# Performance work log

Measured on AMD Instinct MI355X. Metric: run time of the kernel, lower is better.

Reference implementation:

```python
import jax, jax.numpy as jnp
import numpy as np

B, S, HID = 2, 1024, 4096
H, KV, D = 32, 8, 128
EPS = 1e-6
ROPE_THETA = 1000000.0


def _make_freqs_cis(seq_len, head_dim, theta):
    inv_freq = 1.0 / (theta ** (jnp.arange(0, head_dim, 2, dtype=jnp.float32) / head_dim))
    ang = jnp.arange(seq_len, dtype=jnp.float32)[:, None] * inv_freq[None, :]  # [S, D/2]
    emb = jnp.concatenate([ang, ang], axis=-1)                                 # [S, D]
    cos, sin = jnp.cos(emb), jnp.sin(emb)
    return jnp.stack([cos, sin, -sin], axis=0)                                 # [3, S, D]


def setup_inputs() -> dict:
    key = jax.random.key(0)
    ks = jax.random.split(key, 8)
    scale = 0.02
    return {
        "hidden_states": jax.random.normal(ks[0], (B, S, HID), dtype=jnp.float32),
        "freqs_cis": _make_freqs_cis(S, D, ROPE_THETA),
        "Wq": jax.random.normal(ks[1], (H * D, HID), dtype=jnp.float32) * scale,
        "Wk": jax.random.normal(ks[2], (KV * D, HID), dtype=jnp.float32) * scale,
        "Wv": jax.random.normal(ks[3], (KV * D, HID), dtype=jnp.float32) * scale,
        "Wo": jax.random.normal(ks[4], (HID, H * D), dtype=jnp.float32) * scale,
        "q_norm_w": jnp.ones((D,), jnp.float32) + jax.random.normal(ks[5], (D,), jnp.float32) * scale,
        "k_norm_w": jnp.ones((D,), jnp.float32) + jax.random.normal(ks[6], (D,), jnp.float32) * scale,
    }


def _rmsnorm(x, w):
    # per-head RMSNorm over last dim (rms_norm_add=False -> plain weight multiply)
    return x * jax.lax.rsqrt(jnp.mean(x * x, axis=-1, keepdims=True) + EPS) * w


def _rope(x, cos, sin, nsin):
    # matches apply_rope: e = x*cos; e[:half] += x[half:]*nsin; e[half:] += x[:half]*sin
    half = x.shape[-1] // 2
    e = x * cos
    lo = e[..., :half] + x[..., half:] * nsin[..., :half]
    hi = e[..., half:] + x[..., :half] * sin[..., half:]
    return jnp.concatenate([lo, hi], axis=-1)


def reference(hidden_states, freqs_cis, Wq, Wk, Wv, Wo, q_norm_w, k_norm_w):
    b, s, _ = hidden_states.shape
    # QKV projections (no bias)
    q = jnp.einsum("bsh,oh->bso", hidden_states, Wq).reshape(b, s, H, D).transpose(0, 2, 1, 3)
    k = jnp.einsum("bsh,oh->bso", hidden_states, Wk).reshape(b, s, KV, D).transpose(0, 2, 1, 3)
    v = jnp.einsum("bsh,oh->bso", hidden_states, Wv).reshape(b, s, KV, D).transpose(0, 2, 1, 3)
    # per-head RMSNorm (Qwen3 'gemma3' q/k norms)
    q = _rmsnorm(q, q_norm_w)
    k = _rmsnorm(k, k_norm_w)
    # RoPE
    cos, sin, nsin = freqs_cis[0], freqs_cis[1], freqs_cis[2]  # [S, D] each, broadcast over (b, heads)
    q = _rope(q, cos, sin, nsin)
    k = _rope(k, cos, sin, nsin)
    # GQA: repeat kv heads to match query heads (repeat_interleave dim=1)
    rep = H // KV
    k = jnp.repeat(k, rep, axis=1)
    v = jnp.repeat(v, rep, axis=1)
    # SDPA (no mask, past_key_value=None path)
    scale = D ** -0.5
    attn = jax.nn.softmax(jnp.einsum("bhqd,bhkd->bhqk", q, k) * scale, axis=-1)
    out = jnp.einsum("bhqk,bhkd->bhqd", attn, v)
    out = out.transpose(0, 2, 1, 3).reshape(b, s, H * D)
    return jnp.einsum("bsi,hi->bsh", out, Wo)
```

## Files before the change

kernel.cpp:

```cpp
#include <hip/hip_runtime.h>


typedef __attribute__((ext_vector_type(8))) short s8v;
typedef __attribute__((ext_vector_type(4))) float f4v;
typedef __attribute__((ext_vector_type(8))) unsigned short u8v;
typedef __attribute__((ext_vector_type(4))) float float4v;
typedef __attribute__((ext_vector_type(2))) float float2v;
typedef unsigned short us;

#define SB() __builtin_amdgcn_sched_barrier(0)

__device__ __forceinline__ void BARRIER() {
  asm volatile("" ::: "memory");
  __builtin_amdgcn_s_barrier();
  asm volatile("" ::: "memory");
}

__device__ __forceinline__ us f2b(float f) {
  unsigned u = __builtin_bit_cast(unsigned, f);
  u += 0x7fffu + ((u >> 16) & 1u);
  return (us)(u >> 16);
}
__device__ __forceinline__ float b2f(us h) {
  return __builtin_bit_cast(float, (unsigned)h << 16);
}

__device__ __forceinline__ void gload16(const void* g, void* l) {
  __builtin_amdgcn_global_load_lds(
      (const __attribute__((address_space(1))) unsigned int*)g,
      (__attribute__((address_space(3))) unsigned int*)l, 16, 0, 0);
}

__global__ __launch_bounds__(256) void cvt_all_k(const float* __restrict__ h,
                                                 const float* __restrict__ wq,
                                                 const float* __restrict__ wk,
                                                 const float* __restrict__ wv,
                                                 us* __restrict__ dst) {
  long blk = blockIdx.x;
  const float* src;
  long off;
  if (blk < 4096)        { src = h;  off = 0; }
  else if (blk < 12288)  { src = wq; off = 4096; }
  else if (blk < 14336)  { src = wk; off = 12288; }
  else                   { src = wv; off = 14336; }
  long i = (blk - off) * 2048 + (long)threadIdx.x * 8;
  long o = blk * 2048 + (long)threadIdx.x * 8;
  float4v a = *(const float4v*)(src + i);
  float4v b = *(const float4v*)(src + i + 4);
  u8v v;
  v[0] = f2b(a[0]); v[1] = f2b(a[1]); v[2] = f2b(a[2]); v[3] = f2b(a[3]);
  v[4] = f2b(b[0]); v[5] = f2b(b[1]); v[6] = f2b(b[2]); v[7] = f2b(b[3]);
  *(u8v*)(dst + o) = v;
}

template <int AH, bool F32OUT, bool CVTTAIL>
__global__ __launch_bounds__(512, 2) void gemm8p(const us* __restrict__ A,
                                                 const us* __restrict__ W,
                                                 void* __restrict__ Cv,
                                                 int K, int nkt, int ldc,
                                                 int cm, int cn, int ncn,
                                                 int nGemm,
                                                 const float* __restrict__ csrc,
                                                 us* __restrict__ cdst) {
  if constexpr (CVTTAIL) {
    if ((int)blockIdx.x >= nGemm) {
      long c = (long)((int)blockIdx.x - nGemm) * 512 + threadIdx.x;
      for (; c < 2097152; c += 64 * 512) {
        long i = c * 8;
        float4v x = *(const float4v*)(csrc + i);
        float4v y = *(const float4v*)(csrc + i + 4);
        u8v v;
        v[0] = f2b(x[0]); v[1] = f2b(x[1]); v[2] = f2b(x[2]); v[3] = f2b(x[3]);
        v[4] = f2b(y[0]); v[5] = f2b(y[1]); v[6] = f2b(y[2]); v[7] = f2b(y[3]);
        *(u8v*)(cdst + i) = v;
      }
      return;
    }
  }

  constexpr int FR = AH / 32;
  constexpr int LA = AH / 64;
  constexpr int VM = 2 * LA + 2;

  __shared__ __align__(16) us Ah[2][2][AH * 64];
  __shared__ __align__(16) us Bh[2][2][128 * 64];
  const int tid = threadIdx.x, lane = tid & 63, w = tid >> 6;
  const int wr = w >> 2, wc = w & 3;
  const int lr = lane & 15, lg = lane >> 4;

  const int xcd = (int)blockIdx.x & 7;
  const int i2 = (int)blockIdx.x >> 3;
  const int im = i2 % cm, itn = i2 / cm;
  const long m0 = (long)((xcd / ncn) * cm + im) * (2 * AH);
  const long n0 = (long)((xcd % ncn) * cn + itn) * 256;

  const int rA0 = tid >> 3;
  const int sc0 = ((tid & 7) ^ (rA0 & 7)) << 3;

#define STGH(dst, src, LOADS)                                           \
  do {                                                                  \
    const us* _s = (src);                                               \
    us* _d = (dst);                                                     \
    _Pragma("unroll") for (int l = 0; l < (LOADS); ++l)                 \
      gload16(_s + (long)(rA0 + l * 64) * K + sc0, _d + (l * 512 + tid) * 8); \
  } while (0)

  const us* Asrc = A + m0 * K;
  const us* Bsrc = W + n0 * K;
  const long hKA = (long)AH * K;
  const long hKB = (long)128 * K;

  const int ra = wr * (AH / 2) + lr, rb = wc * 32 + lr;
  const int offA0 = ra * 64 + ((lg ^ (ra & 7)) << 3);
  const int offA1 = ra * 64 + (((4 + lg) ^ (ra & 7)) << 3);
  const int offB0 = rb * 64 + ((lg ^ (rb & 7)) << 3);
  const int offB1 = rb * 64 + (((4 + lg) ^ (rb & 7)) << 3);

  f4v acc[2 * FR][4];
#pragma unroll
  for (int i = 0; i < 2 * FR; ++i)
#pragma unroll
    for (int j = 0; j < 4; ++j) acc[i][j] = (f4v){0.f, 0.f, 0.f, 0.f};

  const int nk = nkt;

  STGH(Ah[0][0], Asrc, LA);
  STGH(Bh[0][0], Bsrc, 2);
  STGH(Bh[0][1], Bsrc + hKB, 2);
  STGH(Ah[0][1], Asrc + hKA, LA);
  STGH(Ah[1][0], Asrc + 64, LA);
  STGH(Bh[1][1], Bsrc + hKB + 64, 2);
  STGH(Ah[1][1], Asrc + hKA + 64, LA);
  asm volatile("s_waitcnt vmcnt(%0)" :: "i"(VM) : "memory");
  BARRIER();

  s8v a[FR][2], b0[2][2], b1[2][2];

#define RD_A(H)                                                         \
  _Pragma("unroll") for (int f = 0; f < FR; ++f) {                      \
    a[f][0] = *(const s8v*)(&Ah[d][H][offA0 + f * 1024]);               \
    a[f][1] = *(const s8v*)(&Ah[d][H][offA1 + f * 1024]);               \
  }
#define RD_B(BB, H)                                                     \
  _Pragma("unroll") for (int g = 0; g < 2; ++g) {                       \
    BB[g][0] = *(const s8v*)(&Bh[d][H][offB0 + g * 1024]);              \
    BB[g][1] = *(const s8v*)(&Bh[d][H][offB1 + g * 1024]);              \
  }
#define QUAD(QM, QN, BB)                                                \
  __builtin_amdgcn_s_setprio(1);                                        \
  _Pragma("unroll") for (int f = 0; f < FR; ++f)                        \
  _Pragma("unroll") for (int g = 0; g < 2; ++g) {                       \
    f4v t = acc[QM * FR + f][QN * 2 + g];                               \
    t = __builtin_amdgcn_mfma_f32_16x16x32_bf16(a[f][0], BB[g][0], t, 0, 0, 0); \
    t = __builtin_amdgcn_mfma_f32_16x16x32_bf16(a[f][1], BB[g][1], t, 0, 0, 0); \
    acc[QM * FR + f][QN * 2 + g] = t;                                   \
  }                                                                     \
  __builtin_amdgcn_s_setprio(0);
#define PREMFMA()                                                       \
  BARRIER();                                                            \
  asm volatile("s_waitcnt lgkmcnt(0)" ::: "memory");                    \
  SB();

  for (int kt = 0; kt < nk; ++kt) {
    const int d = kt & 1;
    const long kb2 = (long)(kt + 2) * 64;
    const bool p1 = (kt + 1 < nk), p2 = (kt + 2 < nk);

    RD_A(0)
    RD_B(b0, 0)
    if (p1) STGH(Bh[d ^ 1][0], Bsrc + (long)(kt + 1) * 64, 2);
    PREMFMA()
    QUAD(0, 0, b0)
    SB(); BARRIER();

    RD_B(b1, 1)
    if (p2) STGH(Ah[d][0], Asrc + kb2, LA);
    PREMFMA()
    QUAD(0, 1, b1)
    SB(); BARRIER();

    RD_A(1)
    if (p2) STGH(Bh[d][1], Bsrc + hKB + kb2, 2);
    PREMFMA()
    QUAD(1, 1, b1)
    SB(); BARRIER();

    if (p2) STGH(Ah[d][1], Asrc + hKA + kb2, LA);
    PREMFMA()
    QUAD(1, 0, b0)
    SB();
    if (p2) asm volatile("s_waitcnt vmcnt(%0)" :: "i"(VM) : "memory");
    else    asm volatile("s_waitcnt vmcnt(0)" ::: "memory");
    BARRIER();
  }

#pragma unroll
  for (int qm = 0; qm < 2; ++qm)
#pragma unroll
    for (int f = 0; f < FR; ++f) {
      long row = m0 + qm * AH + wr * (AH / 2) + f * 16 + lg * 4;
#pragma unroll
      for (int qn = 0; qn < 2; ++qn)
#pragma unroll
        for (int g = 0; g < 2; ++g) {
          long col = n0 + qn * 128 + wc * 32 + g * 16 + lr;
          f4v v = acc[qm * FR + f][qn * 2 + g];
          if constexpr (F32OUT) {
            float* C = (float*)Cv;
#pragma unroll
            for (int r = 0; r < 4; ++r) C[(row + r) * ldc + col] = v[r];
          } else {
            us* C = (us*)Cv;
#pragma unroll
            for (int r = 0; r < 4; ++r) C[(row + r) * ldc + col] = f2b(v[r]);
          }
        }
    }
#undef STGH
#undef RD_A
#undef RD_B
#undef QUAD
#undef PREMFMA
}

__global__ __launch_bounds__(256) void rms_rope_k(us* __restrict__ qkv,
                                                  const float* __restrict__ fc,
                                                  const float* __restrict__ qw,
                                                  const float* __restrict__ kw) {
  int idx = blockIdx.x * 4 + (threadIdx.x >> 6);
  int lane = threadIdx.x & 63;
  int head = idx % 40;
  int row = idx / 40;
  int s = row & 1023;
  us* p;
  const float* w;
  if (head < 32) { p = qkv + (long)row * 6144 + head * 128; w = qw; }
  else           { p = qkv + (long)row * 6144 + 4096 + (head - 32) * 128; w = kw; }

  unsigned v = ((const unsigned*)p)[lane];
  float x0 = b2f((us)(v & 0xffff)), x1 = b2f((us)(v >> 16));
  float ss = x0 * x0 + x1 * x1;
#pragma unroll
  for (int off = 32; off; off >>= 1) ss += __shfl_xor(ss, off);
  float r = rsqrtf(ss * (1.0f / 128.0f) + 1e-6f);
  float2v wv = ((const float2v*)w)[lane];
  float y0 = x0 * r * wv[0], y1 = x1 * r * wv[1];
  float py0 = __shfl(y0, lane ^ 32);
  float py1 = __shfl(y1, lane ^ 32);
  float2v cv = ((const float2v*)(fc + (long)s * 128))[lane];
  const float* sbase = (lane < 32) ? (fc + 2 * 1024 * 128) : (fc + 1024 * 128);
  float2v sv = ((const float2v*)(sbase + (long)s * 128))[lane];
  float e0 = y0 * cv[0] + py0 * sv[0];
  float e1 = y1 * cv[1] + py1 * sv[1];
  ((unsigned*)p)[lane] = (unsigned)f2b(e0) | ((unsigned)f2b(e1) << 16);
}

__global__ __launch_bounds__(256) void attn_k(const us* __restrict__ qkv,
                                              us* __restrict__ ao) {
  __shared__ us Kt[64 * 128];
  __shared__ us Vt[128 * 72];
  __shared__ us Pl[4 * 1024];

  const int bid = blockIdx.x;
  const int qt = bid & 15;
  const int h = (bid >> 4) & 31;
  const int b = bid >> 9;
  const int kvh = h >> 2;
  const int tid = threadIdx.x, lane = tid & 63, w = tid >> 6;
  const int lr = lane & 15, lg = lane >> 4;

  const us* Qb =
      qkv + (long)(b * 1024 + qt * 64 + w * 16 + lr) * 6144 + h * 128;
  s8v qf[4];
#pragma unroll
  for (int ks = 0; ks < 4; ++ks) qf[ks] = *(const s8v*)(Qb + ks * 32 + lg * 8);

  f4v o[8];
#pragma unroll
  for (int n = 0; n < 8; ++n) o[n] = (f4v){0.f, 0.f, 0.f, 0.f};
  float m[4], l[4];
#pragma unroll
  for (int r = 0; r < 4; ++r) { m[r] = -1e30f; l[r] = 0.f; }

  const float SL = 0.08838834764831845f * 1.4426950408889634f;
  const long krow = (long)b * 1024 * 6144 + 4096 + kvh * 128;
  const long vrow = (long)b * 1024 * 6144 + 5120 + kvh * 128;

  for (int kt = 0; kt < 16; ++kt) {
    __syncthreads();
#pragma unroll
    for (int t = 0; t < 4; ++t) {
      int c = t * 256 + tid;
      int row = c >> 4;
      int sc = (c & 15) ^ (row & 7);
      gload16(qkv + krow + (long)(kt * 64 + row) * 6144 + sc * 8, &Kt[c * 8]);
    }
#pragma unroll
    for (int t = 0; t < 4; ++t) {
      int c = t * 256 + tid;
      int key = c & 63;
      int d0 = (c >> 6) * 8;
      s8v v = *(const s8v*)(qkv + vrow + (long)(kt * 64 + key) * 6144 + d0);
#pragma unroll
      for (int i = 0; i < 8; ++i) Vt[(d0 + i) * 72 + key] = (us)v[i];
    }
    __syncthreads();

    f4v sacc[4];
#pragma unroll
    for (int j = 0; j < 4; ++j) sacc[j] = (f4v){0.f, 0.f, 0.f, 0.f};
    __builtin_amdgcn_s_setprio(1);
#pragma unroll
    for (int ks = 0; ks < 4; ++ks) {
#pragma unroll
      for (int j = 0; j < 4; ++j) {
        int key = j * 16 + lr;
        s8v kf = *(const s8v*)&Kt[key * 128 + (((ks * 64 + lg * 16) ^ ((key & 7) << 4)) >> 1)];
        sacc[j] = __builtin_amdgcn_mfma_f32_16x16x32_bf16(qf[ks], kf, sacc[j], 0, 0, 0);
      }
    }
    __builtin_amdgcn_s_setprio(0);

    float sm[4];
#pragma unroll
    for (int r = 0; r < 4; ++r)
      sm[r] = fmaxf(fmaxf(sacc[0][r], sacc[1][r]), fmaxf(sacc[2][r], sacc[3][r]));
#pragma unroll
    for (int off = 1; off < 16; off <<= 1)
#pragma unroll
      for (int r = 0; r < 4; ++r) sm[r] = fmaxf(sm[r], __shfl_xor(sm[r], off));
    float alpha[4];
#pragma unroll
    for (int r = 0; r < 4; ++r) {
      float nm = fmaxf(m[r], sm[r] * SL);
      alpha[r] = exp2f(m[r] - nm);
      m[r] = nm;
      l[r] *= alpha[r];
    }
#pragma unroll
    for (int n = 0; n < 8; ++n)
#pragma unroll
      for (int r = 0; r < 4; ++r) o[n][r] *= alpha[r];

    us* pw = Pl + w * 1024;
#pragma unroll
    for (int j = 0; j < 4; ++j)
#pragma unroll
      for (int r = 0; r < 4; ++r) {
        float p = exp2f(sacc[j][r] * SL - m[r]);
        l[r] += p;
        int prow = lg * 4 + r, pcol = j * 16 + lr;
        pw[(prow * 128 + ((pcol * 2) ^ ((prow & 7) << 4))) >> 1] = f2b(p);
      }

    __builtin_amdgcn_s_setprio(1);
#pragma unroll
    for (int ks = 0; ks < 2; ++ks) {
      int bo = ks * 64 + lg * 16;
      s8v pf = *(const s8v*)&Pl[w * 1024 + ((lr * 128 + (bo ^ ((lr & 7) << 4))) >> 1)];
#pragma unroll
      for (int n = 0; n < 8; ++n) {
        s8v vf = *(const s8v*)&Vt[(n * 16 + lr) * 72 + ks * 32 + lg * 8];
        o[n] = __builtin_amdgcn_mfma_f32_16x16x32_bf16(pf, vf, o[n], 0, 0, 0);
      }
    }
    __builtin_amdgcn_s_setprio(0);
  }

#pragma unroll
  for (int off = 1; off < 16; off <<= 1)
#pragma unroll
    for (int r = 0; r < 4; ++r) l[r] += __shfl_xor(l[r], off);
  float inv[4];
#pragma unroll
  for (int r = 0; r < 4; ++r) inv[r] = 1.f / l[r];
  const long ob = (long)(b * 1024 + qt * 64 + w * 16) * 4096 + h * 128;
#pragma unroll
  for (int n = 0; n < 8; ++n)
#pragma unroll
    for (int r = 0; r < 4; ++r)
      ao[ob + (long)(lg * 4 + r) * 4096 + n * 16 + lr] = f2b(o[n][r] * inv[r]);
}

extern "C" void kernel_launch(void* const* d_in, const int* in_sizes, int n_in,
                              void* d_out, int out_size, void* d_ws, size_t ws_size,
                              hipStream_t stream) {
  const float* hidden = (const float*)d_in[0];
  const float* fc     = (const float*)d_in[1];
  const float* Wq     = (const float*)d_in[2];
  const float* Wk     = (const float*)d_in[3];
  const float* Wv     = (const float*)d_in[4];
  const float* Wo     = (const float*)d_in[5];
  const float* qw     = (const float*)d_in[6];
  const float* kw     = (const float*)d_in[7];

  us* hb  = (us*)d_ws;
  us* wb  = hb + (long)2048 * 4096;
  us* wbo = wb + (long)6144 * 4096;
  us* qkv = wbo + (long)4096 * 4096;
  us* ao  = qkv + (long)2048 * 6144;

  cvt_all_k<<<16384, 256, 0, stream>>>(hidden, Wq, Wk, Wv, hb);

  gemm8p<128, false, true><<<256, 512, 0, stream>>>(
      hb, wb, qkv, 4096, 64, 6144, 4, 6, 4, 192, Wo, wbo);

  rms_rope_k<<<20480, 256, 0, stream>>>(qkv, fc, qw, kw);

  attn_k<<<1024, 256, 0, stream>>>(qkv, ao);

  gemm8p<64, true, false><<<256, 512, 0, stream>>>(
      ao, wbo, d_out, 4096, 64, 4096, 8, 4, 4, 256, nullptr, nullptr);
}
```

Baseline: 345.2 us.

## Software-pipeline LDS fragment reads across GEMM k-tiles with partial lgkmcnt waits

After: 581.8 us. +68.5%, slower.

```diff
diff --git a/kernel.cpp b/kernel.cpp
--- a/kernel.cpp
+++ b/kernel.cpp
@@ -80,7 +80,6 @@
 
   constexpr int FR = AH / 32;
   constexpr int LA = AH / 64;
-  constexpr int VM = 2 * LA + 2;
 
   __shared__ __align__(16) us Ah[2][2][AH * 64];
   __shared__ __align__(16) us Bh[2][2][128 * 64];
@@ -124,6 +123,31 @@
 
   const int nk = nkt;
 
+  s8v a0[FR][2], a1[FR][2], b0A[2][2], b0B[2][2], b1[2][2];
+
+#define RD_A(AA, D, H)                                                  \
+  _Pragma("unroll") for (int f = 0; f < FR; ++f) {                      \
+    AA[f][0] = *(const s8v*)(&Ah[D][H][offA0 + f * 1024]);              \
+    AA[f][1] = *(const s8v*)(&Ah[D][H][offA1 + f * 1024]);              \
+  }
+#define RD_B(BB, D, H)                                                  \
+  _Pragma("unroll") for (int g = 0; g < 2; ++g) {                       \
+    BB[g][0] = *(const s8v*)(&Bh[D][H][offB0 + g * 1024]);              \
+    BB[g][1] = *(const s8v*)(&Bh[D][H][offB1 + g * 1024]);              \
+  }
+#define QUAD(AA, BB, QM, QN)                                            \
+  __builtin_amdgcn_s_setprio(1);                                        \
+  _Pragma("unroll") for (int f = 0; f < FR; ++f)                        \
+  _Pragma("unroll") for (int g = 0; g < 2; ++g) {                       \
+    f4v t = acc[QM * FR + f][QN * 2 + g];                               \
+    t = __builtin_amdgcn_mfma_f32_16x16x32_bf16(AA[f][0], BB[g][0], t, 0, 0, 0); \
+    t = __builtin_amdgcn_mfma_f32_16x16x32_bf16(AA[f][1], BB[g][1], t, 0, 0, 0); \
+    acc[QM * FR + f][QN * 2 + g] = t;                                   \
+  }                                                                     \
+  __builtin_amdgcn_s_setprio(0);
+#define LGKMW(N) asm volatile("s_waitcnt lgkmcnt(%0)" :: "i"(N) : "memory")
+#define VMCNTW(N) asm volatile("s_waitcnt vmcnt(%0)" :: "i"(N) : "memory")
+
   STGH(Ah[0][0], Asrc, LA);
   STGH(Bh[0][0], Bsrc, 2);
   STGH(Bh[0][1], Bsrc + hKB, 2);
@@ -131,67 +155,56 @@
   STGH(Ah[1][0], Asrc + 64, LA);
   STGH(Bh[1][1], Bsrc + hKB + 64, 2);
   STGH(Ah[1][1], Asrc + hKA + 64, LA);
-  asm volatile("s_waitcnt vmcnt(%0)" :: "i"(VM) : "memory");
+  VMCNTW(2 * LA + 2);
   BARRIER();
-
-  s8v a[FR][2], b0[2][2], b1[2][2];
-
-#define RD_A(H)                                                         \
-  _Pragma("unroll") for (int f = 0; f < FR; ++f) {                      \
-    a[f][0] = *(const s8v*)(&Ah[d][H][offA0 + f * 1024]);               \
-    a[f][1] = *(const s8v*)(&Ah[d][H][offA1 + f * 1024]);               \
-  }
-#define RD_B(BB, H)                                                     \
-  _Pragma("unroll") for (int g = 0; g < 2; ++g) {                       \
-    BB[g][0] = *(const s8v*)(&Bh[d][H][offB0 + g * 1024]);              \
-    BB[g][1] = *(const s8v*)(&Bh[d][H][offB1 + g * 1024]);              \
-  }
-#define QUAD(QM, QN, BB)                                                \
-  __builtin_amdgcn_s_setprio(1);                                        \
-  _Pragma("unroll") for (int f = 0; f < FR; ++f)                        \
-  _Pragma("unroll") for (int g = 0; g < 2; ++g) {                       \
-    f4v t = acc[QM * FR + f][QN * 2 + g];                               \
-    t = __builtin_amdgcn_mfma_f32_16x16x32_bf16(a[f][0], BB[g][0], t, 0, 0, 0); \
-    t = __builtin_amdgcn_mfma_f32_16x16x32_bf16(a[f][1], BB[g][1], t, 0, 0, 0); \
-    acc[QM * FR + f][QN * 2 + g] = t;                                   \
-  }                                                                     \
-  __builtin_amdgcn_s_setprio(0);
-#define PREMFMA()                                                       \
-  BARRIER();                                                            \
-  asm volatile("s_waitcnt lgkmcnt(0)" ::: "memory");                    \
-  SB();
-
-  for (int kt = 0; kt < nk; ++kt) {
-    const int d = kt & 1;
-    const long kb2 = (long)(kt + 2) * 64;
-    const bool p1 = (kt + 1 < nk), p2 = (kt + 2 < nk);
-
-    RD_A(0)
-    RD_B(b0, 0)
-    if (p1) STGH(Bh[d ^ 1][0], Bsrc + (long)(kt + 1) * 64, 2);
-    PREMFMA()
-    QUAD(0, 0, b0)
-    SB(); BARRIER();
-
-    RD_B(b1, 1)
-    if (p2) STGH(Ah[d][0], Asrc + kb2, LA);
-    PREMFMA()
-    QUAD(0, 1, b1)
-    SB(); BARRIER();
-
-    RD_A(1)
-    if (p2) STGH(Bh[d][1], Bsrc + hKB + kb2, 2);
-    PREMFMA()
-    QUAD(1, 1, b1)
-    SB(); BARRIER();
-
-    if (p2) STGH(Ah[d][1], Asrc + hKA + kb2, LA);
-    PREMFMA()
-    QUAD(1, 0, b0)
-    SB();
-    if (p2) asm volatile("s_waitcnt vmcnt(%0)" :: "i"(VM) : "memory");
-    else    asm volatile("s_waitcnt vmcnt(0)" ::: "memory");
-    BARRIER();
+  RD_A(a0, 0, 0);
+  RD_B(b0A, 0, 0);
+
+#define TILE(KT, D, B0CUR, B0NXT)                                       \
+  do {                                                                  \
+    const int kt = (KT);                                                \
+    const long kb2 = (long)(kt + 2) * 64;                               \
+    const bool p1 = (kt + 1 < nk), p2 = (kt + 2 < nk);                  \
+                                        \
+    RD_B(b1, D, 1);                                                     \
+    if (p1) STGH(Bh[(D) ^ 1][0], Bsrc + (long)(kt + 1) * 64, 2);        \
+    BARRIER();                                                          \
+    LGKMW(4); SB();                                                     \
+    QUAD(a0, B0CUR, 0, 0)                                               \
+    SB(); BARRIER();                                                    \
+                                        \
+    RD_A(a1, D, 1);                                                     \
+    if (p2) STGH(Ah[D][0], Asrc + kb2, LA);                             \
+    BARRIER();                                                          \
+    LGKMW(2 * FR); SB();                                                \
+    QUAD(a0, b1, 0, 1)                                                  \
+    SB(); BARRIER();                                                    \
+                                        \
+    if (p2) STGH(Bh[D][1], Bsrc + hKB + kb2, 2);                        \
+    BARRIER();                                                          \
+    LGKMW(0); SB();                                                     \
+    QUAD(a1, b1, 1, 1)                                                  \
+    SB(); BARRIER();                                                    \
+               \
+    if (p2)      { VMCNTW(LA + 2); }                                    \
+    else         { VMCNTW(0); }                                         \
+    if (p2) STGH(Ah[D][1], Asrc + hKA + kb2, LA);                       \
+    BARRIER();                                                          \
+    if (p1) {                                                           \
+      RD_A(a0, (D) ^ 1, 0);                                             \
+      RD_B(B0NXT, (D) ^ 1, 0);                                          \
+      LGKMW(2 * FR + 4);                                                \
+    } else {                                                            \
+      LGKMW(0);                                                         \
+    }                                                                   \
+    SB();                                                               \
+    QUAD(a1, B0CUR, 1, 0)                                               \
+    SB(); BARRIER();                                                    \
+  } while (0)
+
+  for (int kt2 = 0; kt2 < nk; kt2 += 2) {
+    TILE(kt2, 0, b0A, b0B);
+    TILE(kt2 + 1, 1, b0B, b0A);
   }
 
 #pragma unroll
@@ -220,7 +233,9 @@
 #undef RD_A
 #undef RD_B
 #undef QUAD
-#undef PREMFMA
+#undef TILE
+#undef LGKMW
+#undef VMCNTW
 }
 
 __global__ __launch_bounds__(256) void rms_rope_k(us* __restrict__ qkv,
```

## Double-buffer GEMM LDS fragment reads to overlap with MFMA quadrants

Applied to the files above, without the earlier changes.

Result: slower. 379.0 us (+9.8%).

```diff
diff --git a/kernel.cpp b/kernel.cpp
--- a/kernel.cpp
+++ b/kernel.cpp
@@ -54,7 +54,7 @@
 }
 
 template <int AH, bool F32OUT, bool CVTTAIL>
-__global__ __launch_bounds__(512, 2) void gemm8p(const us* __restrict__ A,
+__global__ __launch_bounds__(512, 1) void gemm8p(const us* __restrict__ A,
                                                  const us* __restrict__ W,
                                                  void* __restrict__ Cv,
                                                  int K, int nkt, int ldc,
@@ -80,7 +80,6 @@
 
   constexpr int FR = AH / 32;
   constexpr int LA = AH / 64;
-  constexpr int VM = 2 * LA + 2;
 
   __shared__ __align__(16) us Ah[2][2][AH * 64];
   __shared__ __align__(16) us Bh[2][2][128 * 64];
@@ -124,6 +123,31 @@
 
   const int nk = nkt;
 
+  s8v a0[FR][2], a1[FR][2], b0[2][2], b1[2][2];
+
+#define RD_A(AA, D, H)                                                  \
+  _Pragma("unroll") for (int f = 0; f < FR; ++f) {                      \
+    AA[f][0] = *(const s8v*)(&Ah[D][H][offA0 + f * 1024]);              \
+    AA[f][1] = *(const s8v*)(&Ah[D][H][offA1 + f * 1024]);              \
+  }
+#define RD_B(BB, D, H)                                                  \
+  _Pragma("unroll") for (int g = 0; g < 2; ++g) {                       \
+    BB[g][0] = *(const s8v*)(&Bh[D][H][offB0 + g * 1024]);              \
+    BB[g][1] = *(const s8v*)(&Bh[D][H][offB1 + g * 1024]);              \
+  }
+#define QUAD(AA, BB, QM, QN)                                            \
+  __builtin_amdgcn_s_setprio(1);                                        \
+  _Pragma("unroll") for (int f = 0; f < FR; ++f)                        \
+  _Pragma("unroll") for (int g = 0; g < 2; ++g) {                       \
+    f4v t = acc[QM * FR + f][QN * 2 + g];                               \
+    t = __builtin_amdgcn_mfma_f32_16x16x32_bf16(AA[f][0], BB[g][0], t, 0, 0, 0); \
+    t = __builtin_amdgcn_mfma_f32_16x16x32_bf16(AA[f][1], BB[g][1], t, 0, 0, 0); \
+    acc[QM * FR + f][QN * 2 + g] = t;                                   \
+  }                                                                     \
+  __builtin_amdgcn_s_setprio(0);
+#define LGKMW(N) asm volatile("s_waitcnt lgkmcnt(%0)" :: "i"(N) : "memory")
+#define VMCNTW(N) asm volatile("s_waitcnt vmcnt(%0)" :: "i"(N) : "memory")
+
   STGH(Ah[0][0], Asrc, LA);
   STGH(Bh[0][0], Bsrc, 2);
   STGH(Bh[0][1], Bsrc + hKB, 2);
@@ -131,66 +155,50 @@
   STGH(Ah[1][0], Asrc + 64, LA);
   STGH(Bh[1][1], Bsrc + hKB + 64, 2);
   STGH(Ah[1][1], Asrc + hKA + 64, LA);
-  asm volatile("s_waitcnt vmcnt(%0)" :: "i"(VM) : "memory");
+  VMCNTW(2 * LA + 2);
   BARRIER();
-
-  s8v a[FR][2], b0[2][2], b1[2][2];
-
-#define RD_A(H)                                                         \
-  _Pragma("unroll") for (int f = 0; f < FR; ++f) {                      \
-    a[f][0] = *(const s8v*)(&Ah[d][H][offA0 + f * 1024]);               \
-    a[f][1] = *(const s8v*)(&Ah[d][H][offA1 + f * 1024]);               \
-  }
-#define RD_B(BB, H)                                                     \
-  _Pragma("unroll") for (int g = 0; g < 2; ++g) {                       \
-    BB[g][0] = *(const s8v*)(&Bh[d][H][offB0 + g * 1024]);              \
-    BB[g][1] = *(const s8v*)(&Bh[d][H][offB1 + g * 1024]);              \
-  }
-#define QUAD(QM, QN, BB)                                                \
-  __builtin_amdgcn_s_setprio(1);                                        \
-  _Pragma("unroll") for (int f = 0; f < FR; ++f)                        \
-  _Pragma("unroll") for (int g = 0; g < 2; ++g) {                       \
-    f4v t = acc[QM * FR + f][QN * 2 + g];                               \
-    t = __builtin_amdgcn_mfma_f32_16x16x32_bf16(a[f][0], BB[g][0], t, 0, 0, 0); \
-    t = __builtin_amdgcn_mfma_f32_16x16x32_bf16(a[f][1], BB[g][1], t, 0, 0, 0); \
-    acc[QM * FR + f][QN * 2 + g] = t;                                   \
-  }                                                                     \
-  __builtin_amdgcn_s_setprio(0);
-#define PREMFMA()                                                       \
-  BARRIER();                                                            \
-  asm volatile("s_waitcnt lgkmcnt(0)" ::: "memory");                    \
-  SB();
+  RD_A(a0, 0, 0);
+  RD_B(b0, 0, 0);
 
   for (int kt = 0; kt < nk; ++kt) {
     const int d = kt & 1;
     const long kb2 = (long)(kt + 2) * 64;
     const bool p1 = (kt + 1 < nk), p2 = (kt + 2 < nk);
 
-    RD_A(0)
-    RD_B(b0, 0)
+    RD_B(b1, d, 1);
     if (p1) STGH(Bh[d ^ 1][0], Bsrc + (long)(kt + 1) * 64, 2);
-    PREMFMA()
-    QUAD(0, 0, b0)
+    BARRIER();
+    LGKMW(4); SB();
+    QUAD(a0, b0, 0, 0)
     SB(); BARRIER();
 
-    RD_B(b1, 1)
+    RD_A(a1, d, 1);
     if (p2) STGH(Ah[d][0], Asrc + kb2, LA);
-    PREMFMA()
-    QUAD(0, 1, b1)
+    BARRIER();
+    LGKMW(2 * FR); SB();
+    QUAD(a0, b1, 0, 1)
     SB(); BARRIER();
 
-    RD_A(1)
     if (p2) STGH(Bh[d][1], Bsrc + hKB + kb2, 2);
-    PREMFMA()
-    QUAD(1, 1, b1)
+    BARRIER();
+    LGKMW(0); SB();
+    QUAD(a1, b1, 1, 1)
     SB(); BARRIER();
 
+    if (p2)      { VMCNTW(LA + 2); }
+    else         { VMCNTW(0); }
     if (p2) STGH(Ah[d][1], Asrc + hKA + kb2, LA);
-    PREMFMA()
-    QUAD(1, 0, b0)
+    BARRIER();
+    if (p1) {
+      RD_A(a0, d ^ 1, 0);
+      LGKMW(2 * FR);
+    } else {
+      LGKMW(0);
+    }
     SB();
-    if (p2) asm volatile("s_waitcnt vmcnt(%0)" :: "i"(VM) : "memory");
-    else    asm volatile("s_waitcnt vmcnt(0)" ::: "memory");
+    QUAD(a1, b0, 1, 0)
+    SB();
+    if (p1) RD_B(b0, d ^ 1, 0);
     BARRIER();
   }
 
@@ -220,7 +228,8 @@
 #undef RD_A
 #undef RD_B
 #undef QUAD
-#undef PREMFMA
+#undef LGKMW
+#undef VMCNTW
 }
 
 __global__ __launch_bounds__(256) void rms_rope_k(us* __restrict__ qkv,
```

## Fuse Q RMSNorm+RoPE into attention, pack V transpose stores, relax GEMM sched barriers

Applied to the files above, without the earlier changes.

After: 337.5 us. 1.02x faster.

```diff
diff --git a/kernel.cpp b/kernel.cpp
--- a/kernel.cpp
+++ b/kernel.cpp
@@ -171,24 +171,23 @@
     if (p1) STGH(Bh[d ^ 1][0], Bsrc + (long)(kt + 1) * 64, 2);
     PREMFMA()
     QUAD(0, 0, b0)
-    SB(); BARRIER();
+    BARRIER();
 
     RD_B(b1, 1)
     if (p2) STGH(Ah[d][0], Asrc + kb2, LA);
     PREMFMA()
     QUAD(0, 1, b1)
-    SB(); BARRIER();
+    BARRIER();
 
     RD_A(1)
     if (p2) STGH(Bh[d][1], Bsrc + hKB + kb2, 2);
     PREMFMA()
     QUAD(1, 1, b1)
-    SB(); BARRIER();
+    BARRIER();
 
     if (p2) STGH(Ah[d][1], Asrc + hKA + kb2, LA);
     PREMFMA()
     QUAD(1, 0, b0)
-    SB();
     if (p2) asm volatile("s_waitcnt vmcnt(%0)" :: "i"(VM) : "memory");
     else    asm volatile("s_waitcnt vmcnt(0)" ::: "memory");
     BARRIER();
@@ -225,17 +224,14 @@
 
 __global__ __launch_bounds__(256) void rms_rope_k(us* __restrict__ qkv,
                                                   const float* __restrict__ fc,
-                                                  const float* __restrict__ qw,
                                                   const float* __restrict__ kw) {
   int idx = blockIdx.x * 4 + (threadIdx.x >> 6);
   int lane = threadIdx.x & 63;
-  int head = idx % 40;
-  int row = idx / 40;
+  int head = idx & 7;
+  int row = idx >> 3;
   int s = row & 1023;
-  us* p;
-  const float* w;
-  if (head < 32) { p = qkv + (long)row * 6144 + head * 128; w = qw; }
-  else           { p = qkv + (long)row * 6144 + 4096 + (head - 32) * 128; w = kw; }
+  us* p = qkv + (long)row * 6144 + 4096 + head * 128;
+  const float* w = kw;
 
   unsigned v = ((const unsigned*)p)[lane];
   float x0 = b2f((us)(v & 0xffff)), x1 = b2f((us)(v >> 16));
@@ -256,7 +252,9 @@
 }
 
 __global__ __launch_bounds__(256) void attn_k(const us* __restrict__ qkv,
-                                              us* __restrict__ ao) {
+                                              us* __restrict__ ao,
+                                              const float* __restrict__ fc,
+                                              const float* __restrict__ qw) {
   __shared__ us Kt[64 * 128];
   __shared__ us Vt[128 * 72];
   __shared__ us Pl[4 * 1024];
@@ -269,11 +267,40 @@
   const int tid = threadIdx.x, lane = tid & 63, w = tid >> 6;
   const int lr = lane & 15, lg = lane >> 4;
 
-  const us* Qb =
-      qkv + (long)(b * 1024 + qt * 64 + w * 16 + lr) * 6144 + h * 128;
+  const int srow = qt * 64 + w * 16 + lr;
+  const us* Qb = qkv + (long)(b * 1024 + srow) * 6144 + h * 128;
+  s8v qr[4];
+#pragma unroll
+  for (int ks = 0; ks < 4; ++ks) qr[ks] = *(const s8v*)(Qb + ks * 32 + lg * 8);
+
+  float ssq = 0.f;
+#pragma unroll
+  for (int ks = 0; ks < 4; ++ks)
+#pragma unroll
+    for (int j = 0; j < 8; ++j) {
+      float x = b2f((us)qr[ks][j]);
+      ssq += x * x;
+    }
+  ssq += __shfl_xor(ssq, 16);
+  ssq += __shfl_xor(ssq, 32);
+  const float rr = rsqrtf(ssq * (1.0f / 128.0f) + 1e-6f);
+
+  const float* cosp = fc + (long)srow * 128;
+  const float* sinp = fc + 1024 * 128 + (long)srow * 128;
   s8v qf[4];
 #pragma unroll
-  for (int ks = 0; ks < 4; ++ks) qf[ks] = *(const s8v*)(Qb + ks * 32 + lg * 8);
+  for (int ks = 0; ks < 4; ++ks) {
+    const int d0 = ks * 32 + lg * 8;
+    const int dp = d0 ^ 64;
+    const float sgn = (ks < 2) ? -1.f : 1.f;
+#pragma unroll
+    for (int j = 0; j < 8; ++j) {
+      float y  = b2f((us)qr[ks][j])     * rr * qw[d0 + j];
+      float yp = b2f((us)qr[ks ^ 2][j]) * rr * qw[dp + j];
+      float e = y * cosp[d0 + j] + yp * sgn * sinp[d0 + j];
+      qf[ks][j] = (short)f2b(e);
+    }
+  }
 
   f4v o[8];
 #pragma unroll
@@ -296,13 +323,18 @@
       gload16(qkv + krow + (long)(kt * 64 + row) * 6144 + sc * 8, &Kt[c * 8]);
     }
 #pragma unroll
-    for (int t = 0; t < 4; ++t) {
+    for (int t = 0; t < 2; ++t) {
       int c = t * 256 + tid;
-      int key = c & 63;
-      int d0 = (c >> 6) * 8;
-      s8v v = *(const s8v*)(qkv + vrow + (long)(kt * 64 + key) * 6144 + d0);
-#pragma unroll
-      for (int i = 0; i < 8; ++i) Vt[(d0 + i) * 72 + key] = (us)v[i];
+      int kp = c & 31;
+      int d0 = (c >> 5) * 8;
+      const us* vsrc = qkv + vrow + (long)(kt * 64) * 6144 + d0;
+      s8v va = *(const s8v*)(vsrc + (long)(2 * kp) * 6144);
+      s8v vb = *(const s8v*)(vsrc + (long)(2 * kp + 1) * 6144);
+#pragma unroll
+      for (int i = 0; i < 8; ++i) {
+        unsigned pk = (unsigned)(us)va[i] | ((unsigned)(us)vb[i] << 16);
+        *(unsigned*)&Vt[(d0 + i) * 72 + 2 * kp] = pk;
+      }
     }
     __syncthreads();
 
@@ -405,9 +437,9 @@
   gemm8p<128, false, true><<<256, 512, 0, stream>>>(
       hb, wb, qkv, 4096, 64, 6144, 4, 6, 4, 192, Wo, wbo);
 
-  rms_rope_k<<<20480, 256, 0, stream>>>(qkv, fc, qw, kw);
-
-  attn_k<<<1024, 256, 0, stream>>>(qkv, ao);
+  rms_rope_k<<<4096, 256, 0, stream>>>(qkv, fc, kw);
+
+  attn_k<<<1024, 256, 0, stream>>>(qkv, ao, fc, qw);
 
   gemm8p<64, true, false><<<256, 512, 0, stream>>>(
       ao, wbo, d_out, 4096, 64, 4096, 8, 4, 4, 256, nullptr, nullptr);
```
